# Performance work log

Measured on AMD Instinct MI355X. Metric: run time of the kernel, lower is better.

Reference implementation:

```python
import jax, jax.numpy as jnp
import numpy as np

D_MODEL = 256
NHEAD = 8
NUM_EXPERTS = 5
LQ, LK, BATCH = 100, 1024, 16
LN_EPS = 1e-5


def setup_inputs() -> dict:
    key = jax.random.key(0)
    ks = jax.random.split(key, 12)
    d, E = D_MODEL, NUM_EXPERTS
    s = 1.0 / np.sqrt(d)
    return {
        "tgt": jax.random.normal(ks[0], (LQ, BATCH, d), jnp.float32),
        "memory": jax.random.normal(ks[1], (LK, BATCH, d), jnp.float32),
        "query_pos": jax.random.normal(ks[2], (LQ, BATCH, d), jnp.float32),
        "pos": jax.random.normal(ks[3], (LK, BATCH, d), jnp.float32),
        # per-expert MultiheadAttention params (packed q,k,v in_proj like torch)
        "w_in": jax.random.normal(ks[4], (E, 3 * d, d), jnp.float32) * s,
        "b_in": jnp.zeros((E, 3 * d), jnp.float32),
        "w_out": jax.random.normal(ks[5], (E, d, d), jnp.float32) * s,
        "b_out": jnp.zeros((E, d), jnp.float32),
        # gating network
        "w_gate": jax.random.normal(ks[6], (E, d), jnp.float32) * s,
        "b_gate": jnp.zeros((E,), jnp.float32),
        # LayerNorm
        "ln_gamma": jnp.ones((d,), jnp.float32),
        "ln_beta": jnp.zeros((d,), jnp.float32),
    }


def _moe_cross_attn(tgt, memory, query_pos, pos, w_in, b_in, w_out, b_out,
                    w_gate, b_gate, ln_gamma, ln_beta):
    Lq, B, d = tgt.shape
    H = NHEAD
    hd = d // H
    E = w_in.shape[0]
    Lk = memory.shape[0]

    # gating over (seq*batch, d) -> softmax over experts
    gate = jax.nn.softmax(tgt @ w_gate.T + b_gate, axis=-1)  # (Lq, B, E)

    q_emb = tgt + query_pos      # (Lq, B, d)
    k_emb = memory + pos         # (Lk, B, d)

    wq, wk, wv = w_in[:, :d], w_in[:, d:2 * d], w_in[:, 2 * d:]
    bq, bk, bv = b_in[:, :d], b_in[:, d:2 * d], b_in[:, 2 * d:]

    # batched projections across all experts (replaces python loop of MHA calls)
    q = jnp.einsum('lbd,eod->elbo', q_emb, wq) + bq[:, None, None, :]
    k = jnp.einsum('sbd,eod->esbo', k_emb, wk) + bk[:, None, None, :]
    v = jnp.einsum('sbd,eod->esbo', memory, wv) + bv[:, None, None, :]

    q = q.reshape(E, Lq, B, H, hd) * (1.0 / np.sqrt(hd))
    k = k.reshape(E, Lk, B, H, hd)
    v = v.reshape(E, Lk, B, H, hd)

    scores = jnp.einsum('elbhk,esbhk->ebhls', q, k)      # (E, B, H, Lq, Lk)
    attn = jax.nn.softmax(scores, axis=-1)
    ctx = jnp.einsum('ebhls,esbhk->elbhk', attn, v).reshape(E, Lq, B, d)

    out = jnp.einsum('elbd,eod->elbo', ctx, w_out) + b_out[:, None, None, :]

    # softmax-gated weighted combine of expert outputs
    mo = jnp.einsum('lbe,elbd->lbd', gate, out)

    x = tgt + mo  # dropout is identity (p=0.0)
    mu = jnp.mean(x, axis=-1, keepdims=True)
    var = jnp.var(x, axis=-1, keepdims=True)
    return (x - mu) * jax.lax.rsqrt(var + LN_EPS) * ln_gamma + ln_beta


def reference(tgt, memory, query_pos, pos, w_in, b_in, w_out, b_out,
              w_gate, b_gate, ln_gamma, ln_beta):
    return _moe_cross_attn(tgt, memory, query_pos, pos, w_in, b_in, w_out,
                           b_out, w_gate, b_gate, ln_gamma, ln_beta)
```

## Files before the change

### kernel.cpp

```cpp
#include <hip/hip_runtime.h>


typedef __bf16 bf16x8 __attribute__((ext_vector_type(8)));
typedef float f32x4 __attribute__((ext_vector_type(4)));
typedef unsigned int u32x4 __attribute__((ext_vector_type(4)));
typedef unsigned int u32x2 __attribute__((ext_vector_type(2)));
typedef unsigned short u16x4 __attribute__((ext_vector_type(4)));
typedef unsigned short us;

__device__ __forceinline__ us f2bf(float f) {
    unsigned u = __builtin_bit_cast(unsigned, f);
    u += 0x7FFFu + ((u >> 16) & 1u);
    return (us)(u >> 16);
}

__device__ __forceinline__ float bf2f(us v) {
    unsigned u = ((unsigned)v) << 16;
    return __builtin_bit_cast(float, u);
}

__device__ __forceinline__ bf16x8 ld_bf8(const us* p) {
    return __builtin_bit_cast(bf16x8, *reinterpret_cast<const u32x4*>(p));
}

__device__ __forceinline__ void gld_lds16(const us* g, us* l) {
    __builtin_amdgcn_global_load_lds(
        (const __attribute__((address_space(1))) unsigned int*)g,
        (__attribute__((address_space(3))) unsigned int*)l, 16, 0, 0);
}

__launch_bounds__(256)
__global__ void cvt_all(const float* __restrict__ tgt, const float* __restrict__ qpos,
                        const float* __restrict__ mem, const float* __restrict__ pos,
                        const float* __restrict__ w_in, const float* __restrict__ w_out,
                        us* __restrict__ Aq, us* __restrict__ Ak, us* __restrict__ Av,
                        us* __restrict__ Wb, us* __restrict__ WOb)
{
    const int bid = blockIdx.x;
    const int tid = threadIdx.x;
    if (bid < 400) {
        int i = bid * 256 + tid;
        f32x4 a = reinterpret_cast<const f32x4*>(tgt)[i];
        f32x4 b = reinterpret_cast<const f32x4*>(qpos)[i];
        u16x4 r;
#pragma unroll
        for (int j = 0; j < 4; ++j) r[j] = f2bf(a[j] + b[j]);
        reinterpret_cast<u16x4*>(Aq)[i] = r;
    } else if (bid < 4496) {
        int i = (bid - 400) * 256 + tid;
        f32x4 m = reinterpret_cast<const f32x4*>(mem)[i];
        f32x4 p = reinterpret_cast<const f32x4*>(pos)[i];
        u16x4 rk, rv;
#pragma unroll
        for (int j = 0; j < 4; ++j) { rk[j] = f2bf(m[j] + p[j]); rv[j] = f2bf(m[j]); }
        reinterpret_cast<u16x4*>(Ak)[i] = rk;
        reinterpret_cast<u16x4*>(Av)[i] = rv;
    } else if (bid < 5456) {
        int i = (bid - 4496) * 256 + tid;
        f32x4 a = reinterpret_cast<const f32x4*>(w_in)[i];
        u16x4 r;
#pragma unroll
        for (int j = 0; j < 4; ++j) r[j] = f2bf(a[j]);
        reinterpret_cast<u16x4*>(Wb)[i] = r;
    } else {
        int i = (bid - 5456) * 256 + tid;
        f32x4 a = reinterpret_cast<const f32x4*>(w_out)[i];
        u16x4 r;
#pragma unroll
        for (int j = 0; j < 4; ++j) r[j] = f2bf(a[j]);
        reinterpret_cast<u16x4*>(WOb)[i] = r;
    }
}

template <bool BF16OUT>
__device__ __forceinline__ void gemm_body(const us* __restrict__ A,
                                          const us* __restrict__ W,
                                          const float* __restrict__ bias,
                                          void* __restrict__ Cout,
                                          float scale, int M)
{
    const int row0 = blockIdx.x * 128;
    const int col0 = blockIdx.y * 128;
    __shared__ us As[128 * 64];
    __shared__ us Bs[128 * 64];
    const int tid  = threadIdx.x;
    const int lane = tid & 63;
    const int w    = tid >> 6;
    const int l15  = lane & 15;
    const int quad = lane >> 4;
    const int wm   = (w >> 1) * 64;
    const int wn   = (w & 1) * 64;
    const int srow = lane >> 3;
    const int gofs = ((lane & 7) ^ srow) * 8;

    f32x4 acc[4][4] = {};

    for (int k0 = 0; k0 < 256; k0 += 64) {
        __syncthreads();
#pragma unroll
        for (int cc = 0; cc < 4; ++cc) {
            const int c = w * 4 + cc;
            const int row = c * 8 + srow;
            gld_lds16(A + (size_t)(row0 + row) * 256 + k0 + gofs, &As[c * 512]);
            gld_lds16(W + (size_t)(col0 + row) * 256 + k0 + gofs, &Bs[c * 512]);
        }
        __syncthreads();
#pragma unroll
        for (int kh = 0; kh < 2; ++kh) {
            bf16x8 af[4], bf[4];
#pragma unroll
            for (int mi = 0; mi < 4; ++mi) {
                const int row = wm + mi * 16 + l15;
                const int seg = (kh * 4 + quad) ^ (row & 7);
                af[mi] = ld_bf8(&As[row * 64 + seg * 8]);
            }
#pragma unroll
            for (int ni = 0; ni < 4; ++ni) {
                const int col = wn + ni * 16 + l15;
                const int seg = (kh * 4 + quad) ^ (col & 7);
                bf[ni] = ld_bf8(&Bs[col * 64 + seg * 8]);
            }
#pragma unroll
            for (int mi = 0; mi < 4; ++mi)
#pragma unroll
                for (int ni = 0; ni < 4; ++ni)
                    acc[mi][ni] = __builtin_amdgcn_mfma_f32_16x16x32_bf16(af[mi], bf[ni], acc[mi][ni], 0, 0, 0);
        }
    }
#pragma unroll
    for (int mi = 0; mi < 4; ++mi) {
#pragma unroll
        for (int ni = 0; ni < 4; ++ni) {
            const int col = col0 + wn + ni * 16 + l15;
            const float bv = bias[col];
#pragma unroll
            for (int r = 0; r < 4; ++r) {
                const int row = row0 + wm + mi * 16 + quad * 4 + r;
                if (row < M) {
                    float v = (acc[mi][ni][r] + bv) * scale;
                    if constexpr (BF16OUT)
                        reinterpret_cast<us*>(Cout)[(size_t)row * 256 + col] = f2bf(v);
                    else
                        reinterpret_cast<float*>(Cout)[(size_t)row * 256 + col] = v;
                }
            }
        }
    }
}

__launch_bounds__(256)
__global__ void gemm_qkv(const us* __restrict__ Aq, const us* __restrict__ Ak,
                         const us* __restrict__ Av, const us* __restrict__ Wb,
                         const float* __restrict__ b_in,
                         us* __restrict__ Qb, us* __restrict__ Kb, us* __restrict__ Vb)
{
    const int z = blockIdx.z;
    if (z < 5) {
        if (blockIdx.x >= 13) return;
        gemm_body<true>(Aq, Wb + (size_t)z * 196608, b_in + (size_t)z * 768,
                        Qb + (size_t)z * 409600, 0.17677669529663687f, 1600);
    } else if (z < 10) {
        const int e = z - 5;
        gemm_body<true>(Ak, Wb + 65536 + (size_t)e * 196608, b_in + (size_t)e * 768 + 256,
                        Kb + (size_t)e * 4194304, 1.0f, 16384);
    } else {
        const int e = z - 10;
        gemm_body<true>(Av, Wb + 131072 + (size_t)e * 196608, b_in + (size_t)e * 768 + 512,
                        Vb + (size_t)e * 4194304, 1.0f, 16384);
    }
}

__launch_bounds__(256)
__global__ void gemm_o(const us* __restrict__ CTXb, const us* __restrict__ WOb,
                       const float* __restrict__ b_out, float* __restrict__ OUTf)
{
    const int e = blockIdx.z;
    gemm_body<false>(CTXb + (size_t)e * 409600, WOb + (size_t)e * 65536,
                     b_out + (size_t)e * 256, OUTf + (size_t)e * 409600, 1.0f, 1600);
}

__device__ __forceinline__ int vrow(int d) { return d * 264 + 8 * (d >> 3); }

__launch_bounds__(512)
__global__ void attn(const us* __restrict__ Qb, const us* __restrict__ Kb,
                     const us* __restrict__ Vb, us* __restrict__ PO,
                     float* __restrict__ PL)
{
    const int h = blockIdx.x;
    const int z = blockIdx.y;
    const int s = blockIdx.z;
    const int e = z >> 4, b = z & 15;
    const int tid  = threadIdx.x;
    const int w    = tid >> 6;
    const int lane = tid & 63;
    const int l15  = lane & 15, quad = lane >> 4;
    __shared__ us Ks[256 * 32];
    __shared__ us Vs[8464];
    __shared__ us Ps[7][16 * 40];

    const int key0 = s * 256;
    {
        const int kl  = lane >> 2;
        const int seg = lane & 3;
        const us* kg = Kb + ((size_t)((e * 1024 + key0 + w * 16 + kl) * 16 + b)) * 256
                          + h * 32 + seg * 8;
        gld_lds16(kg, &Ks[w * 512]);
        gld_lds16(kg + (size_t)128 * 16 * 256, &Ks[4096 + w * 512]);

        const int kv = tid >> 2;
        const int sg = tid & 3;
        const us* vg = Vb + ((size_t)((e * 1024 + key0 + kv) * 16 + b)) * 256
                          + h * 32 + sg * 8;
        u32x4 v0 = *reinterpret_cast<const u32x4*>(vg);
        u32x4 v1 = *reinterpret_cast<const u32x4*>(vg + (size_t)128 * 16 * 256);
#pragma unroll
        for (int j = 0; j < 4; ++j) {
            const int d0 = sg * 8 + 2 * j;
            const int e0 = vrow(d0);
            const int e1 = e0 + 264;
            Vs[e0 + kv]       = (us)(v0[j] & 0xffff);
            Vs[e1 + kv]       = (us)(v0[j] >> 16);
            Vs[e0 + 128 + kv] = (us)(v1[j] & 0xffff);
            Vs[e1 + 128 + kv] = (us)(v1[j] >> 16);
        }
    }
    u32x4 qraw = {0u, 0u, 0u, 0u};
    if (w < 7) {
        const int l = w * 16 + l15;
        if (l < 100)
            qraw = *reinterpret_cast<const u32x4*>(
                Qb + ((size_t)((e * 100 + l) * 16 + b)) * 256 + h * 32 + quad * 8);
    }
    const bf16x8 qf = __builtin_bit_cast(bf16x8, qraw);

    __syncthreads();

    if (w >= 7) return;

    const f32x4 zacc = {};
    f32x4 o0 = {}, o1 = {};
    float lsum = 0.0f;

    for (int c = 0; c < 8; ++c) {
        bf16x8 kf0 = ld_bf8(&Ks[(c * 32 + l15) * 32 + quad * 8]);
        bf16x8 kf1 = ld_bf8(&Ks[(c * 32 + 16 + l15) * 32 + quad * 8]);
        f32x4 s0 = __builtin_amdgcn_mfma_f32_16x16x32_bf16(kf0, qf, zacc, 0, 0, 0);
        f32x4 s1 = __builtin_amdgcn_mfma_f32_16x16x32_bf16(kf1, qf, zacc, 0, 0, 0);
        float p0[4], p1[4];
#pragma unroll
        for (int r = 0; r < 4; ++r) {
            p0[r] = __expf(s0[r]);
            p1[r] = __expf(s1[r]);
            lsum += p0[r] + p1[r];
        }
        u32x2 w0, w1;
        w0[0] = (unsigned)f2bf(p0[0]) | ((unsigned)f2bf(p0[1]) << 16);
        w0[1] = (unsigned)f2bf(p0[2]) | ((unsigned)f2bf(p0[3]) << 16);
        w1[0] = (unsigned)f2bf(p1[0]) | ((unsigned)f2bf(p1[1]) << 16);
        w1[1] = (unsigned)f2bf(p1[2]) | ((unsigned)f2bf(p1[3]) << 16);
        *reinterpret_cast<u32x2*>(&Ps[w][l15 * 40 + quad * 4])      = w0;
        *reinterpret_cast<u32x2*>(&Ps[w][l15 * 40 + 16 + quad * 4]) = w1;
        bf16x8 pf  = ld_bf8(&Ps[w][l15 * 40 + quad * 8]);
        bf16x8 vf0 = ld_bf8(&Vs[vrow(l15) + c * 32 + quad * 8]);
        bf16x8 vf1 = ld_bf8(&Vs[vrow(16 + l15) + c * 32 + quad * 8]);
        o0 = __builtin_amdgcn_mfma_f32_16x16x32_bf16(pf, vf0, o0, 0, 0, 0);
        o1 = __builtin_amdgcn_mfma_f32_16x16x32_bf16(pf, vf1, o1, 0, 0, 0);
    }

    lsum += __shfl_xor(lsum, 16, 64);
    lsum += __shfl_xor(lsum, 32, 64);

#pragma unroll
    for (int r = 0; r < 4; ++r) {
        const int row = w * 16 + quad * 4 + r;
        if (row < 100) {
            const size_t o = (((size_t)((s * 5 + e) * 100 + row)) * 16 + b) * 256 + h * 32;
            PO[o + l15]      = f2bf(o0[r]);
            PO[o + 16 + l15] = f2bf(o1[r]);
        }
    }
    const int q = w * 16 + l15;
    if (quad == 0 && q < 100)
        PL[((((size_t)s * 5 + e) * 16 + b) * 8 + h) * 128 + q] = lsum;
}

__launch_bounds__(256)
__global__ void combine(const us* __restrict__ PO, const float* __restrict__ PL,
                        us* __restrict__ CTX)
{
    const int blk = blockIdx.x;
    const int e   = blk / 1600;
    const int rem = blk - e * 1600;
    const int row = rem >> 4;
    const int b   = rem & 15;
    const int d   = threadIdx.x;
    const int h   = d >> 5;
    float O = 0.0f, L = 0.0f;
#pragma unroll
    for (int s = 0; s < 4; ++s) {
        O += bf2f(PO[(((size_t)((s * 5 + e) * 100 + row)) * 16 + b) * 256 + d]);
        L += PL[((((size_t)s * 5 + e) * 16 + b) * 8 + h) * 128 + row];
    }
    CTX[(((size_t)(e * 100 + row)) * 16 + b) * 256 + d] = f2bf(O / L);
}

__launch_bounds__(256)
__global__ void finalize(const float* __restrict__ tgt, const float* __restrict__ w_gate,
                         const float* __restrict__ b_gate, const float* __restrict__ OUTf,
                         const float* __restrict__ gamma, const float* __restrict__ beta,
                         float* __restrict__ out)
{
    const int row = blockIdx.x;
    const int d = threadIdx.x;
    __shared__ float red[4];
    const float t = tgt[(size_t)row * 256 + d];

    float g[5];
#pragma unroll
    for (int e = 0; e < 5; ++e) {
        float part = t * w_gate[e * 256 + d];
#pragma unroll
        for (int off = 32; off >= 1; off >>= 1) part += __shfl_xor(part, off, 64);
        if ((d & 63) == 0) red[d >> 6] = part;
        __syncthreads();
        g[e] = red[0] + red[1] + red[2] + red[3] + b_gate[e];
        __syncthreads();
    }
    float mx = g[0];
#pragma unroll
    for (int e = 1; e < 5; ++e) mx = fmaxf(mx, g[e]);
    float sm = 0.0f;
#pragma unroll
    for (int e = 0; e < 5; ++e) { g[e] = __expf(g[e] - mx); sm += g[e]; }
    const float invs = 1.0f / sm;

    float mo = 0.0f;
#pragma unroll
    for (int e = 0; e < 5; ++e)
        mo += g[e] * invs * OUTf[((size_t)e * 1600 + row) * 256 + d];
    const float x = t + mo;

    float part = x;
#pragma unroll
    for (int off = 32; off >= 1; off >>= 1) part += __shfl_xor(part, off, 64);
    if ((d & 63) == 0) red[d >> 6] = part;
    __syncthreads();
    const float mean = (red[0] + red[1] + red[2] + red[3]) * (1.0f / 256.0f);
    __syncthreads();

    const float diff = x - mean;
    part = diff * diff;
#pragma unroll
    for (int off = 32; off >= 1; off >>= 1) part += __shfl_xor(part, off, 64);
    if ((d & 63) == 0) red[d >> 6] = part;
    __syncthreads();
    const float var = (red[0] + red[1] + red[2] + red[3]) * (1.0f / 256.0f);

    out[(size_t)row * 256 + d] = diff * rsqrtf(var + 1e-5f) * gamma[d] + beta[d];
}

extern "C" void kernel_launch(void* const* d_in, const int* in_sizes, int n_in,
                              void* d_out, int out_size, void* d_ws, size_t ws_size,
                              hipStream_t stream)
{
    const float* tgt    = (const float*)d_in[0];
    const float* mem    = (const float*)d_in[1];
    const float* qpos   = (const float*)d_in[2];
    const float* pos    = (const float*)d_in[3];
    const float* w_in   = (const float*)d_in[4];
    const float* b_in   = (const float*)d_in[5];
    const float* w_out  = (const float*)d_in[6];
    const float* b_out  = (const float*)d_in[7];
    const float* w_gate = (const float*)d_in[8];
    const float* b_gate = (const float*)d_in[9];
    const float* ln_g   = (const float*)d_in[10];
    const float* ln_b   = (const float*)d_in[11];
    float* out = (float*)d_out;

    char* p = (char*)d_ws;
    auto alloc = [&](size_t n) { char* r = p; p += (n + 255) & ~(size_t)255; return r; };

    us* Aq   = (us*)alloc(409600ull * 2);
    us* Ak   = (us*)alloc(4194304ull * 2);
    us* Av   = (us*)alloc(4194304ull * 2);
    us* Wb   = (us*)alloc(983040ull * 2);
    us* WOb  = (us*)alloc(327680ull * 2);
    us* Qb   = (us*)alloc(5ull * 409600 * 2);
    us* Kb   = (us*)alloc(5ull * 4194304 * 2);
    us* Vb   = (us*)alloc(5ull * 4194304 * 2);
    us* CTXb = (us*)alloc(5ull * 409600 * 2);
    float* OUTf = (float*)alloc(5ull * 409600 * 4);
    us*    PO = (us*)d_ws;
    float* PL = (float*)((char*)d_ws + 16384000);

    cvt_all<<<5776, 256, 0, stream>>>(tgt, qpos, mem, pos, w_in, w_out,
                                      Aq, Ak, Av, Wb, WOb);

    gemm_qkv<<<dim3(128, 2, 15), 256, 0, stream>>>(Aq, Ak, Av, Wb, b_in, Qb, Kb, Vb);

    attn<<<dim3(8, 80, 4), 512, 0, stream>>>(Qb, Kb, Vb, PO, PL);

    combine<<<8000, 256, 0, stream>>>(PO, PL, CTXb);

    gemm_o<<<dim3(13, 2, 5), 256, 0, stream>>>(CTXb, WOb, b_out, OUTf);

    finalize<<<1600, 256, 0, stream>>>(tgt, w_gate, b_gate, OUTf, ln_g, ln_b, out);
}
```

Baseline: 220.2 us.

## Double-buffer GEMM LDS tiles and vectorize epilogue via swapped MFMA operands

The shared GEMM body now uses two LDS buffers, so the global-to-LDS load of the next K tile is issued while MFMAs run on the current tile, and one barrier per iteration is dropped. The MFMA operands are swapped so each lane holds four consecutive output columns, which lets the epilogue do one vectorized bias load and packed 8- or 16-byte stores instead of scalar ones. This doubles LDS use per block, which may lower occupancy.

Result: faster. 214.5 us (-2.6%).

```diff
diff --git a/kernel.cpp b/kernel.cpp
--- a/kernel.cpp
+++ b/kernel.cpp
@@ -81,8 +81,8 @@
 {
     const int row0 = blockIdx.x * 128;
     const int col0 = blockIdx.y * 128;
-    __shared__ us As[128 * 64];
-    __shared__ us Bs[128 * 64];
+    __shared__ us As[2 * 8192];
+    __shared__ us Bs[2 * 8192];
     const int tid  = threadIdx.x;
     const int lane = tid & 63;
     const int w    = tid >> 6;
@@ -93,18 +93,31 @@
     const int srow = lane >> 3;
     const int gofs = ((lane & 7) ^ srow) * 8;
 
+#pragma unroll
+    for (int cc = 0; cc < 4; ++cc) {
+        const int c = w * 4 + cc;
+        const int row = c * 8 + srow;
+        gld_lds16(A + (size_t)(row0 + row) * 256 + gofs, &As[c * 512]);
+        gld_lds16(W + (size_t)(col0 + row) * 256 + gofs, &Bs[c * 512]);
+    }
+    __syncthreads();
+
     f32x4 acc[4][4] = {};
 
-    for (int k0 = 0; k0 < 256; k0 += 64) {
-        __syncthreads();
-#pragma unroll
-        for (int cc = 0; cc < 4; ++cc) {
-            const int c = w * 4 + cc;
-            const int row = c * 8 + srow;
-            gld_lds16(A + (size_t)(row0 + row) * 256 + k0 + gofs, &As[c * 512]);
-            gld_lds16(W + (size_t)(col0 + row) * 256 + k0 + gofs, &Bs[c * 512]);
-        }
-        __syncthreads();
+#pragma unroll
+    for (int kt = 0; kt < 4; ++kt) {
+        const int cur = (kt & 1) * 8192;
+        if (kt < 3) {
+            const int nxt = ((kt + 1) & 1) * 8192;
+            const int k0 = (kt + 1) * 64;
+#pragma unroll
+            for (int cc = 0; cc < 4; ++cc) {
+                const int c = w * 4 + cc;
+                const int row = c * 8 + srow;
+                gld_lds16(A + (size_t)(row0 + row) * 256 + k0 + gofs, &As[nxt + c * 512]);
+                gld_lds16(W + (size_t)(col0 + row) * 256 + k0 + gofs, &Bs[nxt + c * 512]);
+            }
+        }
 #pragma unroll
         for (int kh = 0; kh < 2; ++kh) {
             bf16x8 af[4], bf[4];
@@ -112,36 +125,43 @@
             for (int mi = 0; mi < 4; ++mi) {
                 const int row = wm + mi * 16 + l15;
                 const int seg = (kh * 4 + quad) ^ (row & 7);
-                af[mi] = ld_bf8(&As[row * 64 + seg * 8]);
+                af[mi] = ld_bf8(&As[cur + row * 64 + seg * 8]);
             }
 #pragma unroll
             for (int ni = 0; ni < 4; ++ni) {
                 const int col = wn + ni * 16 + l15;
                 const int seg = (kh * 4 + quad) ^ (col & 7);
-                bf[ni] = ld_bf8(&Bs[col * 64 + seg * 8]);
+                bf[ni] = ld_bf8(&Bs[cur + col * 64 + seg * 8]);
             }
 #pragma unroll
             for (int mi = 0; mi < 4; ++mi)
 #pragma unroll
                 for (int ni = 0; ni < 4; ++ni)
-                    acc[mi][ni] = __builtin_amdgcn_mfma_f32_16x16x32_bf16(af[mi], bf[ni], acc[mi][ni], 0, 0, 0);
-        }
-    }
-#pragma unroll
-    for (int mi = 0; mi < 4; ++mi) {
-#pragma unroll
-        for (int ni = 0; ni < 4; ++ni) {
-            const int col = col0 + wn + ni * 16 + l15;
-            const float bv = bias[col];
-#pragma unroll
-            for (int r = 0; r < 4; ++r) {
-                const int row = row0 + wm + mi * 16 + quad * 4 + r;
-                if (row < M) {
-                    float v = (acc[mi][ni][r] + bv) * scale;
-                    if constexpr (BF16OUT)
-                        reinterpret_cast<us*>(Cout)[(size_t)row * 256 + col] = f2bf(v);
-                    else
-                        reinterpret_cast<float*>(Cout)[(size_t)row * 256 + col] = v;
+                    acc[mi][ni] = __builtin_amdgcn_mfma_f32_16x16x32_bf16(bf[ni], af[mi], acc[mi][ni], 0, 0, 0);
+        }
+        if (kt < 3) __syncthreads();
+    }
+
+#pragma unroll
+    for (int ni = 0; ni < 4; ++ni) {
+        const int colb = col0 + wn + ni * 16 + quad * 4;
+        const f32x4 b4 = *reinterpret_cast<const f32x4*>(bias + colb);
+#pragma unroll
+        for (int mi = 0; mi < 4; ++mi) {
+            const int row = row0 + wm + mi * 16 + l15;
+            if (row < M) {
+                if constexpr (BF16OUT) {
+                    u32x2 pk;
+                    pk[0] = (unsigned)f2bf((acc[mi][ni][0] + b4[0]) * scale)
+                          | ((unsigned)f2bf((acc[mi][ni][1] + b4[1]) * scale) << 16);
+                    pk[1] = (unsigned)f2bf((acc[mi][ni][2] + b4[2]) * scale)
+                          | ((unsigned)f2bf((acc[mi][ni][3] + b4[3]) * scale) << 16);
+                    *reinterpret_cast<u32x2*>(reinterpret_cast<us*>(Cout) + (size_t)row * 256 + colb) = pk;
+                } else {
+                    f32x4 v;
+#pragma unroll
+                    for (int r = 0; r < 4; ++r) v[r] = (acc[mi][ni][r] + b4[r]) * scale;
+                    *reinterpret_cast<f32x4*>(reinterpret_cast<float*>(Cout) + (size_t)row * 256 + colb) = v;
                 }
             }
         }
```
